# Performance work log

Measured on AMD Instinct MI355X. Metric: run time of the kernel, lower is better.

Reference implementation:

```python
import jax, jax.numpy as jnp
import numpy as np

EPS = 1e-12  # F.normalize default eps


def setup_inputs() -> dict:
    key = jax.random.key(0)
    k1, k2, k3, k4 = jax.random.split(key, 4)
    b, n, c, h = 8, 4096, 768, 8
    scale = 1.0 / np.sqrt(c)
    return {
        "x": jax.random.normal(k1, (b, n, c), dtype=jnp.float32),
        "W_qkv": jax.random.normal(k2, (c, 3 * c), dtype=jnp.float32) * scale,
        "W_proj": jax.random.normal(k3, (c, c), dtype=jnp.float32) * scale,
        "b_proj": jax.random.normal(k4, (c,), dtype=jnp.float32) * 0.01,
        "temperature": jnp.ones((h, 1, 1), dtype=jnp.float32),
    }


def _l2norm(t):
    # F.normalize(t, dim=-1): t / max(||t||_2, eps)
    nrm = jnp.sqrt(jnp.sum(t * t, axis=-1, keepdims=True))
    return t / jnp.maximum(nrm, EPS)


def reference(x, W_qkv, W_proj, b_proj, temperature):
    b, n, c = x.shape
    h = temperature.shape[0]
    d = c // h  # head_dim
    # qkv: (b, n, 3c) -> (b, n, 3, h, d) -> (3, b, h, d, n)
    qkv = (x @ W_qkv).reshape(b, n, 3, h, d).transpose(2, 0, 3, 4, 1)
    q, k, v = qkv[0], qkv[1], qkv[2]  # each (b, h, d, n)
    qn = _l2norm(q)
    kn = _l2norm(k)
    # cross-covariance attention: (b, h, d, d)
    attn = jnp.einsum('bhdn,bhen->bhde', qn, kn) * temperature
    attn = jax.nn.softmax(attn, axis=-1)
    out = jnp.einsum('bhde,bhen->bhdn', attn, v)  # (b, h, d, n)
    out = out.transpose(0, 3, 1, 2).reshape(b, n, c)
    return out @ W_proj + b_proj
```

## Files before the change

### kernel.cpp

```cpp
#include <hip/hip_runtime.h>
#include <math.h>

#define NB  8
#define SEQ 4096
#define CH  768
#define NH  8
#define HD  96
#define NC3 2304

typedef _Float16 f16x8 __attribute__((ext_vector_type(8)));
typedef float    f32x4 __attribute__((ext_vector_type(4)));

static const size_t XT_B   = 0;
static const size_t UT_B   = 0;
static const size_t ATT_B  = 28311552;
static const size_t MT_B   = 29491200;
static const size_t PT_B   = 38928384;
static const size_t GP_B   = 50331648;
static const size_t XH_B   = 50331648;
static const size_t WH_B   = 100663296;
static const size_t WT_B   = 104202240;
static const size_t WPT_B  = 107741184;
static const size_t G_B    = 108920832;
static const size_t INV_B  = 118358016;

__device__ __forceinline__ void gload16(const void* g, void* l) {
  __builtin_amdgcn_global_load_lds(
      (const __attribute__((address_space(1))) void*)g,
      (__attribute__((address_space(3))) void*)l, 16, 0, 0);
}

__global__ void cvt_f16_kernel(const float* __restrict__ in,
                               _Float16* __restrict__ out, int n4) {
  int i = blockIdx.x * blockDim.x + threadIdx.x;
  if (i < n4) {
    float4 v = *(const float4*)(in + (size_t)i * 4);
    _Float16* o = out + (size_t)i * 4;
    o[0] = (_Float16)v.x; o[1] = (_Float16)v.y;
    o[2] = (_Float16)v.z; o[3] = (_Float16)v.w;
  }
}

__global__ void transpose_cvt_kernel(const float* __restrict__ in,
                                     _Float16* __restrict__ outT,
                                     int R, int C, long sIn, long sOut) {
  __shared__ float t[32][33];
  const int b = blockIdx.z;
  const int c0 = blockIdx.x * 32, r0 = blockIdx.y * 32;
  const int tx = threadIdx.x & 31, ty = threadIdx.x >> 5;
  const float* ib = in + (size_t)b * sIn;
  _Float16* ob = outT + (size_t)b * sOut;
#pragma unroll
  for (int k = 0; k < 4; ++k)
    t[ty + 8 * k][tx] = ib[(size_t)(r0 + ty + 8 * k) * C + c0 + tx];
  __syncthreads();
#pragma unroll
  for (int k = 0; k < 4; ++k)
    ob[(size_t)(c0 + ty + 8 * k) * R + r0 + tx] = (_Float16)t[tx][ty + 8 * k];
}

template<bool FP16OUT, bool BIAS, bool TRI>
__global__ __launch_bounds__(256) void gemm_bt_mfma(
    const _Float16* __restrict__ Ap, const _Float16* __restrict__ Bp,
    const float* __restrict__ bias, void* __restrict__ Cp,
    int K, int lda, int ldb, int ldc,
    long sA, long sB, long sC, int zdiv, long aCS, long bCS, long cCS,
    int gx, int gy) {
  __shared__ __align__(16) _Float16 ldsA[2][128 * 32];
  __shared__ __align__(16) _Float16 ldsB[2][128 * 32];

  const int nwg = gridDim.x;
  const int lid = blockIdx.x;
  const int wg = (lid & 7) * (nwg >> 3) + (lid >> 3);
  int bx, by, z;
  if constexpr (TRI) {
    int tt = wg % 21; z = wg / 21;
    int ti = 0, rem = tt;
    while (rem >= 6 - ti) { rem -= 6 - ti; ++ti; }
    by = ti; bx = ti + rem;
  } else {
    bx = wg % gx; int r2 = wg / gx; by = r2 % gy; z = r2 / gy;
  }
  const int bat = z % zdiv, chk = z / zdiv;
  const _Float16* A = Ap + (size_t)bat * sA + (size_t)chk * aCS;
  const _Float16* B = Bp + (size_t)bat * sB + (size_t)chk * bCS;
  const size_t cOff = (size_t)bat * sC + (size_t)chk * cCS;

  const int row0 = by * 128, col0 = bx * 128;
  const int tid = threadIdx.x;
  const int l = tid & 63, w = tid >> 6;
  const int lo = l & 15, hi = l >> 4;
  const int wr = w >> 1, wc = w & 1;

  const int rw = 32 * w;
  const int lr = l >> 2;
  const int ls = l & 3;

  f32x4 acc[4][4];
#pragma unroll
  for (int i = 0; i < 4; ++i)
#pragma unroll
    for (int j = 0; j < 4; ++j)
      acc[i][j] = (f32x4){0.f, 0.f, 0.f, 0.f};

  auto STAGE = [&](int hb, int k0) {
#pragma unroll
    for (int q = 0; q < 2; ++q) {
      const int r = rw + 16 * q + lr;
      const int ck = ls ^ ((r >> 1) & 3);
      gload16(A + (size_t)(row0 + r) * lda + k0 + 8 * ck,
              &ldsA[hb][(rw + 16 * q) * 32]);
      gload16(B + (size_t)(col0 + r) * ldb + k0 + 8 * ck,
              &ldsB[hb][(rw + 16 * q) * 32]);
    }
  };

  STAGE(0, 0);
  const int nt = K / 32;
  int cur = 0;
  for (int t = 0; t < nt; ++t) {
    if (t + 1 < nt) {
      STAGE(cur ^ 1, 32 * (t + 1));
      asm volatile("s_waitcnt vmcnt(4)" : : : "memory");
    } else {
      asm volatile("s_waitcnt vmcnt(0)" : : : "memory");
    }
    __builtin_amdgcn_s_barrier();

    f16x8 a[4], b[4];
#pragma unroll
    for (int mi = 0; mi < 4; ++mi) {
      int Ra = 64 * wr + 16 * mi + lo;
      a[mi] = *(const f16x8*)&ldsA[cur][Ra * 32 + (hi ^ ((Ra >> 1) & 3)) * 8];
    }
#pragma unroll
    for (int ni = 0; ni < 4; ++ni) {
      int Rb = 64 * wc + 16 * ni + lo;
      b[ni] = *(const f16x8*)&ldsB[cur][Rb * 32 + (hi ^ ((Rb >> 1) & 3)) * 8];
    }
#pragma unroll
    for (int mi = 0; mi < 4; ++mi)
#pragma unroll
      for (int ni = 0; ni < 4; ++ni)
        acc[mi][ni] = __builtin_amdgcn_mfma_f32_16x16x32_f16(
            a[mi], b[ni], acc[mi][ni], 0, 0, 0);

    __builtin_amdgcn_s_barrier();
    cur ^= 1;
  }

#pragma unroll
  for (int ni = 0; ni < 4; ++ni) {
    const int col = col0 + 64 * wc + 16 * ni + lo;
    float bv = 0.f;
    if constexpr (BIAS) bv = bias[col];
#pragma unroll
    for (int mi = 0; mi < 4; ++mi) {
      const int rowb = row0 + 64 * wr + 16 * mi + 4 * hi;
#pragma unroll
      for (int r = 0; r < 4; ++r) {
        float v = acc[mi][ni][r] + bv;
        if constexpr (FP16OUT)
          ((_Float16*)Cp)[cOff + (size_t)(rowb + r) * ldc + col] = (_Float16)v;
        else
          ((float*)Cp)[cOff + (size_t)(rowb + r) * ldc + col] = v;
      }
    }
  }
}

__global__ void reduce_mirror_kernel(const _Float16* __restrict__ GP,
                                     _Float16* __restrict__ G) {
  const int t = blockIdx.x, b = blockIdx.y;
  int ti = 0, rem = t;
  while (rem >= 6 - ti) { rem -= 6 - ti; ++ti; }
  const int tj = ti + rem;
  const int i0 = ti * 128, j0 = tj * 128;
  const int tx = threadIdx.x & 31, ty = threadIdx.x >> 5;
  __shared__ float lds[32][33];
  const size_t cs = (size_t)NB * CH * CH;
  const _Float16* gp = GP + (size_t)b * CH * CH;
  _Float16* g = G + (size_t)b * CH * CH;

  for (int st = 0; st < 16; ++st) {
    const int sr = i0 + (st >> 2) * 32, sc = j0 + (st & 3) * 32;
    __syncthreads();
#pragma unroll
    for (int k = 0; k < 4; ++k) {
      const int r = ty + 8 * k;
      const size_t off = (size_t)(sr + r) * CH + sc + tx;
      float v = ((float)gp[off] + (float)gp[cs + off]) +
                ((float)gp[2 * cs + off] + (float)gp[3 * cs + off]);
      lds[r][tx] = v;
      g[off] = (_Float16)v;
    }
    if (ti != tj) {
      __syncthreads();
#pragma unroll
      for (int k = 0; k < 4; ++k) {
        const int r = ty + 8 * k;
        g[(size_t)(sc + r) * CH + sr + tx] = (_Float16)lds[tx][r];
      }
    }
  }
}

__global__ void norm_kernel(const _Float16* __restrict__ Ut,
                            const _Float16* __restrict__ Wt,
                            float* __restrict__ INVv) {
  const int z = blockIdx.x;
  const int t = z >> 3;
  const int c = blockIdx.y * 128 + threadIdx.x;
  const _Float16* u = Ut + ((size_t)z * CH + c) * CH;
  const _Float16* wv = Wt + ((size_t)(t * CH + c)) * CH;
  float s = 0.f;
  for (int i = 0; i < CH; i += 8) {
    f16x8 uv = *(const f16x8*)(u + i);
    f16x8 wq = *(const f16x8*)(wv + i);
#pragma unroll
    for (int q = 0; q < 8; ++q) s += (float)uv[q] * (float)wq[q];
  }
  s = fmaxf(s, 0.f);
  INVv[(size_t)z * CH + c] = 1.0f / fmaxf(sqrtf(s), 1e-12f);
}

__global__ __launch_bounds__(256) void sattn_kernel(
    const _Float16* __restrict__ WT_, const _Float16* __restrict__ UT_,
    const float* __restrict__ INVv, const float* __restrict__ temp,
    _Float16* __restrict__ ATt) {
  const int bh = blockIdx.x;
  const int b = bh >> 3, h = bh & 7;
  __shared__ __align__(16) _Float16 lds[2][192 * 32];
  __shared__ float S[96][100];

  const int tid = threadIdx.x;
  const int l = tid & 63, w = tid >> 6;
  const int lo = l & 15, hi = l >> 4;
  const int wr = w >> 1, wc = w & 1;
  const int lr = l >> 2, lq = l & 3;

  const _Float16* Abase = WT_ + (size_t)(h * HD) * CH;
  const _Float16* Bbase = UT_ + ((size_t)(8 + b) * CH + h * HD) * CH;

  f32x4 acc[3][3];
#pragma unroll
  for (int i = 0; i < 3; ++i)
#pragma unroll
    for (int j = 0; j < 3; ++j)
      acc[i][j] = (f32x4){0.f, 0.f, 0.f, 0.f};

  auto STAGE = [&](int hb, int k0) {
#pragma unroll
    for (int c = 0; c < 3; ++c) {
      const int group = w * 3 + c;
      const int row = group * 16 + lr;
      const int ck = lq ^ ((row >> 1) & 3);
      const _Float16* src = (row < 96)
          ? Abase + (size_t)row * CH + k0 + 8 * ck
          : Bbase + (size_t)(row - 96) * CH + k0 + 8 * ck;
      gload16(src, &lds[hb][group * 512]);
    }
  };

  STAGE(0, 0);
  int cur = 0;
  for (int t = 0; t < 24; ++t) {
    if (t + 1 < 24) {
      STAGE(cur ^ 1, 32 * (t + 1));
      asm volatile("s_waitcnt vmcnt(3)" : : : "memory");
    } else {
      asm volatile("s_waitcnt vmcnt(0)" : : : "memory");
    }
    __builtin_amdgcn_s_barrier();

    f16x8 a[3], bb[3];
#pragma unroll
    for (int mi = 0; mi < 3; ++mi) {
      const int Ra = 48 * wr + 16 * mi + lo;
      a[mi] = *(const f16x8*)&lds[cur][Ra * 32 + (hi ^ ((Ra >> 1) & 3)) * 8];
    }
#pragma unroll
    for (int ni = 0; ni < 3; ++ni) {
      const int Rb = 96 + 48 * wc + 16 * ni + lo;
      bb[ni] = *(const f16x8*)&lds[cur][Rb * 32 + (hi ^ ((Rb >> 1) & 3)) * 8];
    }
#pragma unroll
    for (int mi = 0; mi < 3; ++mi)
#pragma unroll
      for (int ni = 0; ni < 3; ++ni)
        acc[mi][ni] = __builtin_amdgcn_mfma_f32_16x16x32_f16(
            a[mi], bb[ni], acc[mi][ni], 0, 0, 0);

    __builtin_amdgcn_s_barrier();
    cur ^= 1;
  }

  const float tv = temp[h];
  const float* iq = INVv + (size_t)b * CH + h * HD;
  const float* ik = INVv + (size_t)(8 + b) * CH + h * HD;
#pragma unroll
  for (int ni = 0; ni < 3; ++ni) {
    const int col = 48 * wc + 16 * ni + lo;
    const float ikv = ik[col];
#pragma unroll
    for (int mi = 0; mi < 3; ++mi) {
      const int rb = 48 * wr + 16 * mi + 4 * hi;
#pragma unroll
      for (int r = 0; r < 4; ++r)
        S[rb + r][col] = acc[mi][ni][r] * iq[rb + r] * ikv * tv;
    }
  }
  __syncthreads();

  const int g16 = tid >> 4, l16 = tid & 15;
  _Float16* ab = ATt + (size_t)bh * 9216;
#pragma unroll
  for (int it = 0; it < 6; ++it) {
    const int d = g16 + 16 * it;
    float v[6];
    float mx = -INFINITY;
#pragma unroll
    for (int j = 0; j < 6; ++j) { v[j] = S[d][l16 * 6 + j]; mx = fmaxf(mx, v[j]); }
#pragma unroll
    for (int m = 1; m < 16; m <<= 1) mx = fmaxf(mx, __shfl_xor(mx, m, 16));
    float sum = 0.f;
#pragma unroll
    for (int j = 0; j < 6; ++j) { v[j] = __expf(v[j] - mx); sum += v[j]; }
#pragma unroll
    for (int m = 1; m < 16; m <<= 1) sum += __shfl_xor(sum, m, 16);
    const float inv = 1.0f / sum;
#pragma unroll
    for (int j = 0; j < 6; ++j)
      ab[(size_t)(l16 * 6 + j) * 96 + d] = (_Float16)(v[j] * inv);
  }
}

__global__ void mt_kernel(const _Float16* __restrict__ Wpt,
                          const _Float16* __restrict__ ATt,
                          _Float16* __restrict__ Mt) {
  const int j0 = blockIdx.x * 128;
  const int bh = blockIdx.y;
  const int b = bh >> 3, h = bh & 7;
  const int tx = threadIdx.x & 15, ty = threadIdx.x >> 4;
  __shared__ float Ws[16][128], Ats[16][96];
  float acc[8][6] = {};

  for (int d0 = 0; d0 < 96; d0 += 16) {
    {
      int jj = threadIdx.x >> 1, s8 = (threadIdx.x & 1) * 8;
      f16x8 v = *(const f16x8*)(Wpt + (size_t)(j0 + jj) * CH + h * HD + d0 + s8);
#pragma unroll
      for (int q = 0; q < 8; ++q) Ws[s8 + q][jj] = (float)v[q];
    }
    if (threadIdx.x < 192) {
      int e = threadIdx.x >> 1, s8 = (threadIdx.x & 1) * 8;
      f16x8 v = *(const f16x8*)(ATt + (size_t)bh * 9216 + (size_t)e * 96 + d0 + s8);
#pragma unroll
      for (int q = 0; q < 8; ++q) Ats[s8 + q][e] = (float)v[q];
    }
    __syncthreads();
#pragma unroll
    for (int kk = 0; kk < 16; ++kk) {
      float a[8], bb[6];
#pragma unroll
      for (int i = 0; i < 8; ++i) a[i] = Ws[kk][ty * 8 + i];
#pragma unroll
      for (int j = 0; j < 6; ++j) bb[j] = Ats[kk][tx * 6 + j];
#pragma unroll
      for (int i = 0; i < 8; ++i)
#pragma unroll
        for (int j = 0; j < 6; ++j)
          acc[i][j] += a[i] * bb[j];
    }
    __syncthreads();
  }

  _Float16* mb = Mt + (size_t)b * CH * CH;
#pragma unroll
  for (int i = 0; i < 8; ++i)
#pragma unroll
    for (int j = 0; j < 6; ++j)
      mb[(size_t)(j0 + ty * 8 + i) * CH + h * HD + tx * 6 + j] = (_Float16)acc[i][j];
}

extern "C" void kernel_launch(void* const* d_in, const int* in_sizes, int n_in,
                              void* d_out, int out_size, void* d_ws, size_t ws_size,
                              hipStream_t stream) {
  const float* x      = (const float*)d_in[0];
  const float* W_qkv  = (const float*)d_in[1];
  const float* W_proj = (const float*)d_in[2];
  const float* b_proj = (const float*)d_in[3];
  const float* temp   = (const float*)d_in[4];
  float* out = (float*)d_out;
  char* ws = (char*)d_ws;

  _Float16* XT  = (_Float16*)(ws + XT_B);
  _Float16* UT  = (_Float16*)(ws + UT_B);
  _Float16* ATT = (_Float16*)(ws + ATT_B);
  _Float16* MT  = (_Float16*)(ws + MT_B);
  _Float16* PT  = (_Float16*)(ws + PT_B);
  _Float16* GP  = (_Float16*)(ws + GP_B);
  _Float16* XH  = (_Float16*)(ws + XH_B);
  _Float16* WH  = (_Float16*)(ws + WH_B);
  _Float16* WT  = (_Float16*)(ws + WT_B);
  _Float16* WPT = (_Float16*)(ws + WPT_B);
  _Float16* G   = (_Float16*)(ws + G_B);
  float*    INV = (float*)   (ws + INV_B);

  const long CC = (long)CH * CH;
  const long SC = (long)SEQ * CH;

  cvt_f16_kernel<<<(CH * NC3 / 4 + 255) / 256, 256, 0, stream>>>(
      W_qkv, WH, CH * NC3 / 4);
  transpose_cvt_kernel<<<dim3(CH / 32, SEQ / 32, NB), 256, 0, stream>>>(
      x, XT, SEQ, CH, SC, SC);
  transpose_cvt_kernel<<<dim3(NC3 / 32, CH / 32, 1), 256, 0, stream>>>(
      W_qkv, WT, CH, NC3, 0, 0);
  transpose_cvt_kernel<<<dim3(CH / 32, CH / 32, 1), 256, 0, stream>>>(
      W_proj, WPT, CH, CH, 0, 0);

  gemm_bt_mfma<true, false, true><<<672, 256, 0, stream>>>(
      XT, XT, nullptr, GP, 1024, SEQ, SEQ, CH,
      (long)CH * SEQ, (long)CH * SEQ, CC, NB, 1024, 1024, (long)NB * CC,
      21, 1);

  reduce_mirror_kernel<<<dim3(21, NB), 256, 0, stream>>>(GP, G);

  gemm_bt_mfma<true, false, false><<<576, 256, 0, stream>>>(
      WT, G, nullptr, UT, CH, CH, CH, CH,
      0, CC, CC, NB, CC, 0, (long)NB * CC, 6, 6);

  norm_kernel<<<dim3(16, 6), 128, 0, stream>>>(UT, WT, INV);

  sattn_kernel<<<64, 256, 0, stream>>>(WT, UT, INV, temp, ATT);

  mt_kernel<<<dim3(6, 64), 256, 0, stream>>>(WPT, ATT, MT);

  gemm_bt_mfma<true, false, false><<<288, 256, 0, stream>>>(
      MT, WH + 2 * CH, nullptr, PT, CH, CH, NC3, CH,
      CC, 0, CC, NB, 0, 0, 0, 6, 6);

  cvt_f16_kernel<<<(int)(NB * SC / 4 / 256), 256, 0, stream>>>(
      x, XH, (int)(NB * SC / 4));

  gemm_bt_mfma<false, true, false><<<1536, 256, 0, stream>>>(
      XH, PT, b_proj, out, CH, CH, CH, CH,
      SC, CC, SC, NB, 0, 0, 0, 6, 32);
}
```

Before: 265.2 us.

## Add 256x256 MFMA GEMM tile and fuse fp16 copy of x into transpose

Adds a 512-thread GEMM kernel with 256x256 output tiles and K=64 stages. Its loads for the next stage are interleaved with MFMA sub-blocks inside one tile, and it replaces the 128x128 kernel for the Gram, U and final projection GEMMs. The reduce_mirror triangle tiling is adjusted to match. When the workspace is large enough, the transpose kernel also writes a row-major fp16 copy of x, which removes the separate conversion pass over x. Larger tiles improve operand reuse but give far fewer workgroups (192, 144 and 384), which risks underfilling the GPU's compute units and raises register pressure.

```diff
diff --git a/kernel.cpp b/kernel.cpp
--- a/kernel.cpp
+++ b/kernel.cpp
@@ -23,6 +23,8 @@
 static const size_t WPT_B  = 107741184;
 static const size_t G_B    = 108920832;
 static const size_t INV_B  = 118358016;
+static const size_t XH2_B  = 118407168;
+static const size_t XH_BYTES = (size_t)NB * SEQ * CH * 2;
 
 __device__ __forceinline__ void gload16(const void* g, void* l) {
   __builtin_amdgcn_global_load_lds(
@@ -43,6 +45,7 @@
 
 __global__ void transpose_cvt_kernel(const float* __restrict__ in,
                                      _Float16* __restrict__ outT,
+                                     _Float16* __restrict__ outH,
                                      int R, int C, long sIn, long sOut) {
   __shared__ float t[32][33];
   const int b = blockIdx.z;
@@ -51,8 +54,12 @@
   const float* ib = in + (size_t)b * sIn;
   _Float16* ob = outT + (size_t)b * sOut;
 #pragma unroll
-  for (int k = 0; k < 4; ++k)
-    t[ty + 8 * k][tx] = ib[(size_t)(r0 + ty + 8 * k) * C + c0 + tx];
+  for (int k = 0; k < 4; ++k) {
+    float v = ib[(size_t)(r0 + ty + 8 * k) * C + c0 + tx];
+    t[ty + 8 * k][tx] = v;
+    if (outH)
+      outH[(size_t)b * sOut + (size_t)(r0 + ty + 8 * k) * C + c0 + tx] = (_Float16)v;
+  }
   __syncthreads();
 #pragma unroll
   for (int k = 0; k < 4; ++k)
@@ -60,7 +67,175 @@
 }
 
 template<bool FP16OUT, bool BIAS, bool TRI>
-__global__ __launch_bounds__(256) void gemm_bt_mfma(
+__global__ __launch_bounds__(512) void gemm_bt_256(
+    const _Float16* __restrict__ Ap, const _Float16* __restrict__ Bp,
+    const float* __restrict__ bias, void* __restrict__ Cp,
+    int K, int lda, int ldb, int ldc,
+    long sA, long sB, long sC, int zdiv, long aCS, long bCS, long cCS,
+    int gx, int gy) {
+  __shared__ __align__(16) _Float16 lds[2][2][256 * 64];
+
+  const int nwg = gridDim.x;
+  const int lid = blockIdx.x;
+  const int wg = (lid & 7) * (nwg >> 3) + (lid >> 3);
+  int bx, by, z;
+  if constexpr (TRI) {
+    const int ntri = gx * (gx + 1) / 2;
+    int tt = wg % ntri; z = wg / ntri;
+    int ti = 0, rem = tt;
+    while (rem >= gx - ti) { rem -= gx - ti; ++ti; }
+    by = ti; bx = ti + rem;
+  } else {
+    bx = wg % gx; int r2 = wg / gx; by = r2 % gy; z = r2 / gy;
+  }
+  const int bat = z % zdiv, chk = z / zdiv;
+  const _Float16* A = Ap + (size_t)bat * sA + (size_t)chk * aCS;
+  const _Float16* B = Bp + (size_t)bat * sB + (size_t)chk * bCS;
+  const size_t cOff = (size_t)bat * sC + (size_t)chk * cCS;
+
+  const int row0 = by * 256, col0 = bx * 256;
+  const int tid = threadIdx.x;
+  const int l = tid & 63, w = tid >> 6;
+  const int lo = l & 15, hi = l >> 4;
+  const int wr = w >> 2, wc = w & 3;
+
+  const int srow = l >> 3;
+  const int sslot = l & 7;
+
+  f32x4 acc[8][4];
+#pragma unroll
+  for (int i = 0; i < 8; ++i)
+#pragma unroll
+    for (int j = 0; j < 4; ++j)
+      acc[i][j] = (f32x4){0.f, 0.f, 0.f, 0.f};
+
+  auto STAGE_A = [&](int buf, int k0, int c) {
+    const int r = 32 * w + 8 * c + srow;
+    const int ck = sslot ^ (r & 7);
+    gload16(A + (size_t)(row0 + r) * lda + k0 + 8 * ck,
+            &lds[buf][0][(32 * w + 8 * c) * 64]);
+  };
+  auto STAGE_B = [&](int buf, int k0, int c) {
+    const int r = 32 * w + 8 * c + srow;
+    const int ck = sslot ^ (r & 7);
+    gload16(B + (size_t)(col0 + r) * ldb + k0 + 8 * ck,
+            &lds[buf][1][(32 * w + 8 * c) * 64]);
+  };
+  auto LDA_f = [&](int buf, int mi, int kk) -> f16x8 {
+    const int R = 128 * wr + 16 * mi + lo;
+    const int sl = (kk * 4 + hi) ^ (R & 7);
+    return *(const f16x8*)&lds[buf][0][R * 64 + sl * 8];
+  };
+  auto LDB_f = [&](int buf, int ni, int kk) -> f16x8 {
+    const int R = 64 * wc + 16 * ni + lo;
+    const int sl = (kk * 4 + hi) ^ (R & 7);
+    return *(const f16x8*)&lds[buf][1][R * 64 + sl * 8];
+  };
+
+#pragma unroll
+  for (int c = 0; c < 4; ++c) STAGE_A(0, 0, c);
+#pragma unroll
+  for (int c = 0; c < 4; ++c) STAGE_B(0, 0, c);
+  asm volatile("s_waitcnt vmcnt(0)" ::: "memory");
+  __builtin_amdgcn_s_barrier();
+
+  const int nt = K / 64;
+  int cur = 0;
+  f16x8 a[4][2], b0[2][2], b1[2][2];
+
+  for (int t = 0; t < nt; ++t) {
+    const int nx = cur ^ 1;
+    const bool pre = (t + 1 < nt);
+    const int k1 = 64 * (t + 1);
+
+#pragma unroll
+    for (int mi = 0; mi < 4; ++mi) {
+      a[mi][0] = LDA_f(cur, mi, 0); a[mi][1] = LDA_f(cur, mi, 1);
+    }
+#pragma unroll
+    for (int ni = 0; ni < 2; ++ni) {
+      b0[ni][0] = LDB_f(cur, ni, 0); b0[ni][1] = LDB_f(cur, ni, 1);
+    }
+    if (pre) { STAGE_A(nx, k1, 0); STAGE_A(nx, k1, 1); }
+    __builtin_amdgcn_s_barrier();
+#pragma unroll
+    for (int mi = 0; mi < 4; ++mi)
+#pragma unroll
+      for (int ni = 0; ni < 2; ++ni)
+#pragma unroll
+        for (int kk = 0; kk < 2; ++kk)
+          acc[mi][ni] = __builtin_amdgcn_mfma_f32_16x16x32_f16(
+              a[mi][kk], b0[ni][kk], acc[mi][ni], 0, 0, 0);
+    __builtin_amdgcn_s_barrier();
+
+#pragma unroll
+    for (int ni = 0; ni < 2; ++ni) {
+      b1[ni][0] = LDB_f(cur, ni + 2, 0); b1[ni][1] = LDB_f(cur, ni + 2, 1);
+    }
+    if (pre) { STAGE_A(nx, k1, 2); STAGE_A(nx, k1, 3); }
+    __builtin_amdgcn_s_barrier();
+#pragma unroll
+    for (int mi = 0; mi < 4; ++mi)
+#pragma unroll
+      for (int ni = 0; ni < 2; ++ni)
+#pragma unroll
+        for (int kk = 0; kk < 2; ++kk)
+          acc[mi][ni + 2] = __builtin_amdgcn_mfma_f32_16x16x32_f16(
+              a[mi][kk], b1[ni][kk], acc[mi][ni + 2], 0, 0, 0);
+    __builtin_amdgcn_s_barrier();
+
+#pragma unroll
+    for (int mi = 0; mi < 4; ++mi) {
+      a[mi][0] = LDA_f(cur, mi + 4, 0); a[mi][1] = LDA_f(cur, mi + 4, 1);
+    }
+    if (pre) { STAGE_B(nx, k1, 0); STAGE_B(nx, k1, 1); }
+    __builtin_amdgcn_s_barrier();
+#pragma unroll
+    for (int mi = 0; mi < 4; ++mi)
+#pragma unroll
+      for (int ni = 0; ni < 2; ++ni)
+#pragma unroll
+        for (int kk = 0; kk < 2; ++kk)
+          acc[mi + 4][ni] = __builtin_amdgcn_mfma_f32_16x16x32_f16(
+              a[mi][kk], b0[ni][kk], acc[mi + 4][ni], 0, 0, 0);
+    __builtin_amdgcn_s_barrier();
+
+    if (pre) { STAGE_B(nx, k1, 2); STAGE_B(nx, k1, 3); }
+#pragma unroll
+    for (int mi = 0; mi < 4; ++mi)
+#pragma unroll
+      for (int ni = 0; ni < 2; ++ni)
+#pragma unroll
+        for (int kk = 0; kk < 2; ++kk)
+          acc[mi + 4][ni + 2] = __builtin_amdgcn_mfma_f32_16x16x32_f16(
+              a[mi][kk], b1[ni][kk], acc[mi + 4][ni + 2], 0, 0, 0);
+    asm volatile("s_waitcnt vmcnt(0)" ::: "memory");
+    __builtin_amdgcn_s_barrier();
+    cur = nx;
+  }
+
+#pragma unroll
+  for (int ni = 0; ni < 4; ++ni) {
+    const int col = col0 + 64 * wc + 16 * ni + lo;
+    float bv = 0.f;
+    if constexpr (BIAS) bv = bias[col];
+#pragma unroll
+    for (int mi = 0; mi < 8; ++mi) {
+      const int rowb = row0 + 128 * wr + 16 * mi + 4 * hi;
+#pragma unroll
+      for (int r = 0; r < 4; ++r) {
+        float v = acc[mi][ni][r] + bv;
+        if constexpr (FP16OUT)
+          ((_Float16*)Cp)[cOff + (size_t)(rowb + r) * ldc + col] = (_Float16)v;
+        else
+          ((float*)Cp)[cOff + (size_t)(rowb + r) * ldc + col] = v;
+      }
+    }
+  }
+}
+
+template<bool FP16OUT, bool BIAS>
+__global__ __launch_bounds__(256) void gemm_bt_128(
     const _Float16* __restrict__ Ap, const _Float16* __restrict__ Bp,
     const float* __restrict__ bias, void* __restrict__ Cp,
     int K, int lda, int ldb, int ldc,
@@ -72,15 +247,7 @@
   const int nwg = gridDim.x;
   const int lid = blockIdx.x;
   const int wg = (lid & 7) * (nwg >> 3) + (lid >> 3);
-  int bx, by, z;
-  if constexpr (TRI) {
-    int tt = wg % 21; z = wg / 21;
-    int ti = 0, rem = tt;
-    while (rem >= 6 - ti) { rem -= 6 - ti; ++ti; }
-    by = ti; bx = ti + rem;
-  } else {
-    bx = wg % gx; int r2 = wg / gx; by = r2 % gy; z = r2 / gy;
-  }
+  int bx = wg % gx; int r2 = wg / gx; int by = r2 % gy; int z = r2 / gy;
   const int bat = z % zdiv, chk = z / zdiv;
   const _Float16* A = Ap + (size_t)bat * sA + (size_t)chk * aCS;
   const _Float16* B = Bp + (size_t)bat * sB + (size_t)chk * bCS;
@@ -91,7 +258,6 @@
   const int l = tid & 63, w = tid >> 6;
   const int lo = l & 15, hi = l >> 4;
   const int wr = w >> 1, wc = w & 1;
-
   const int rw = 32 * w;
   const int lr = l >> 2;
   const int ls = l & 3;
@@ -121,9 +287,9 @@
   for (int t = 0; t < nt; ++t) {
     if (t + 1 < nt) {
       STAGE(cur ^ 1, 32 * (t + 1));
-      asm volatile("s_waitcnt vmcnt(4)" : : : "memory");
+      asm volatile("s_waitcnt vmcnt(4)" ::: "memory");
     } else {
-      asm volatile("s_waitcnt vmcnt(0)" : : : "memory");
+      asm volatile("s_waitcnt vmcnt(0)" ::: "memory");
     }
     __builtin_amdgcn_s_barrier();
 
@@ -173,17 +339,17 @@
                                      _Float16* __restrict__ G) {
   const int t = blockIdx.x, b = blockIdx.y;
   int ti = 0, rem = t;
-  while (rem >= 6 - ti) { rem -= 6 - ti; ++ti; }
+  while (rem >= 3 - ti) { rem -= 3 - ti; ++ti; }
   const int tj = ti + rem;
-  const int i0 = ti * 128, j0 = tj * 128;
+  const int i0 = ti * 256, j0 = tj * 256;
   const int tx = threadIdx.x & 31, ty = threadIdx.x >> 5;
   __shared__ float lds[32][33];
   const size_t cs = (size_t)NB * CH * CH;
   const _Float16* gp = GP + (size_t)b * CH * CH;
   _Float16* g = G + (size_t)b * CH * CH;
 
-  for (int st = 0; st < 16; ++st) {
-    const int sr = i0 + (st >> 2) * 32, sc = j0 + (st & 3) * 32;
+  for (int st = 0; st < 64; ++st) {
+    const int sr = i0 + (st >> 3) * 32, sc = j0 + (st & 7) * 32;
     __syncthreads();
 #pragma unroll
     for (int k = 0; k < 4; ++k) {
@@ -267,9 +433,9 @@
   for (int t = 0; t < 24; ++t) {
     if (t + 1 < 24) {
       STAGE(cur ^ 1, 32 * (t + 1));
-      asm volatile("s_waitcnt vmcnt(3)" : : : "memory");
+      asm volatile("s_waitcnt vmcnt(3)" ::: "memory");
     } else {
-      asm volatile("s_waitcnt vmcnt(0)" : : : "memory");
+      asm volatile("s_waitcnt vmcnt(0)" ::: "memory");
     }
     __builtin_amdgcn_s_barrier();
 
@@ -407,28 +573,31 @@
   _Float16* G   = (_Float16*)(ws + G_B);
   float*    INV = (float*)   (ws + INV_B);
 
+  const bool fast = ws_size >= XH2_B + XH_BYTES;
+  _Float16* XHU = fast ? (_Float16*)(ws + XH2_B) : XH;
+
   const long CC = (long)CH * CH;
   const long SC = (long)SEQ * CH;
 
   cvt_f16_kernel<<<(CH * NC3 / 4 + 255) / 256, 256, 0, stream>>>(
       W_qkv, WH, CH * NC3 / 4);
   transpose_cvt_kernel<<<dim3(CH / 32, SEQ / 32, NB), 256, 0, stream>>>(
-      x, XT, SEQ, CH, SC, SC);
+      x, XT, fast ? XHU : nullptr, SEQ, CH, SC, SC);
   transpose_cvt_kernel<<<dim3(NC3 / 32, CH / 32, 1), 256, 0, stream>>>(
-      W_qkv, WT, CH, NC3, 0, 0);
+      W_qkv, WT, nullptr, CH, NC3, 0, 0);
   transpose_cvt_kernel<<<dim3(CH / 32, CH / 32, 1), 256, 0, stream>>>(
-      W_proj, WPT, CH, CH, 0, 0);
-
-  gemm_bt_mfma<true, false, true><<<672, 256, 0, stream>>>(
+      W_proj, WPT, nullptr, CH, CH, 0, 0);
+
+  gemm_bt_256<true, false, true><<<192, 512, 0, stream>>>(
       XT, XT, nullptr, GP, 1024, SEQ, SEQ, CH,
       (long)CH * SEQ, (long)CH * SEQ, CC, NB, 1024, 1024, (long)NB * CC,
-      21, 1);
-
-  reduce_mirror_kernel<<<dim3(21, NB), 256, 0, stream>>>(GP, G);
-
-  gemm_bt_mfma<true, false, false><<<576, 256, 0, stream>>>(
+      3, 1);
+
+  reduce_mirror_kernel<<<dim3(6, NB), 256, 0, stream>>>(GP, G);
+
+  gemm_bt_256<true, false, false><<<144, 512, 0, stream>>>(
       WT, G, nullptr, UT, CH, CH, CH, CH,
-      0, CC, CC, NB, CC, 0, (long)NB * CC, 6, 6);
+      0, CC, CC, NB, CC, 0, (long)NB * CC, 3, 3);
 
   norm_kernel<<<dim3(16, 6), 128, 0, stream>>>(UT, WT, INV);
 
@@ -436,14 +605,15 @@
 
   mt_kernel<<<dim3(6, 64), 256, 0, stream>>>(WPT, ATT, MT);
 
-  gemm_bt_mfma<true, false, false><<<288, 256, 0, stream>>>(
+  gemm_bt_128<true, false><<<288, 256, 0, stream>>>(
       MT, WH + 2 * CH, nullptr, PT, CH, CH, NC3, CH,
       CC, 0, CC, NB, 0, 0, 0, 6, 6);
 
-  cvt_f16_kernel<<<(int)(NB * SC / 4 / 256), 256, 0, stream>>>(
-      x, XH, (int)(NB * SC / 4));
-
-  gemm_bt_mfma<false, true, false><<<1536, 256, 0, stream>>>(
-      XH, PT, b_proj, out, CH, CH, CH, CH,
-      SC, CC, SC, NB, 0, 0, 0, 6, 32);
-}
+  if (!fast)
+    cvt_f16_kernel<<<(int)(NB * SC / 4 / 256), 256, 0, stream>>>(
+        x, XH, (int)(NB * SC / 4));
+
+  gemm_bt_256<false, true, false><<<384, 512, 0, stream>>>(
+      XHU, PT, b_proj, out, CH, CH, CH, CH,
+      SC, CC, SC, NB, 0, 0, 0, 3, 16);
+}
```

After: 307.9 us. 16.1% more time.

## Fuse x fp16 conversion into transpose and add 256-row wide GEMM tiles

Applied to the files above, without the earlier changes.

The transpose kernel for x now also writes a row-major fp16 copy into a separate workspace region, so the standalone fp16 conversion pass over x can be skipped when the workspace is large enough. A new 512-thread GEMM variant with 256x128 tiles replaces the 128x128 kernel for the U and final projection GEMMs. This halves the workgroup count and reuses each B tile across more rows. The wide tiles raise LDS use per workgroup, and the fast path depends on the workspace size.

```diff
diff --git a/kernel.cpp b/kernel.cpp
--- a/kernel.cpp
+++ b/kernel.cpp
@@ -23,6 +23,8 @@
 static const size_t WPT_B  = 107741184;
 static const size_t G_B    = 108920832;
 static const size_t INV_B  = 118358016;
+static const size_t XH2_B  = 118407168;
+static const size_t XH_BYTES = (size_t)NB * SEQ * CH * 2;
 
 __device__ __forceinline__ void gload16(const void* g, void* l) {
   __builtin_amdgcn_global_load_lds(
@@ -43,6 +45,7 @@
 
 __global__ void transpose_cvt_kernel(const float* __restrict__ in,
                                      _Float16* __restrict__ outT,
+                                     _Float16* __restrict__ outH,
                                      int R, int C, long sIn, long sOut) {
   __shared__ float t[32][33];
   const int b = blockIdx.z;
@@ -51,8 +54,12 @@
   const float* ib = in + (size_t)b * sIn;
   _Float16* ob = outT + (size_t)b * sOut;
 #pragma unroll
-  for (int k = 0; k < 4; ++k)
-    t[ty + 8 * k][tx] = ib[(size_t)(r0 + ty + 8 * k) * C + c0 + tx];
+  for (int k = 0; k < 4; ++k) {
+    float v = ib[(size_t)(r0 + ty + 8 * k) * C + c0 + tx];
+    t[ty + 8 * k][tx] = v;
+    if (outH)
+      outH[(size_t)b * sOut + (size_t)(r0 + ty + 8 * k) * C + c0 + tx] = (_Float16)v;
+  }
   __syncthreads();
 #pragma unroll
   for (int k = 0; k < 4; ++k)
@@ -91,7 +98,6 @@
   const int l = tid & 63, w = tid >> 6;
   const int lo = l & 15, hi = l >> 4;
   const int wr = w >> 1, wc = w & 1;
-
   const int rw = 32 * w;
   const int lr = l >> 2;
   const int ls = l & 3;
@@ -121,9 +127,114 @@
   for (int t = 0; t < nt; ++t) {
     if (t + 1 < nt) {
       STAGE(cur ^ 1, 32 * (t + 1));
-      asm volatile("s_waitcnt vmcnt(4)" : : : "memory");
+      asm volatile("s_waitcnt vmcnt(4)" ::: "memory");
     } else {
-      asm volatile("s_waitcnt vmcnt(0)" : : : "memory");
+      asm volatile("s_waitcnt vmcnt(0)" ::: "memory");
+    }
+    __builtin_amdgcn_s_barrier();
+
+    f16x8 a[4], b[4];
+#pragma unroll
+    for (int mi = 0; mi < 4; ++mi) {
+      int Ra = 64 * wr + 16 * mi + lo;
+      a[mi] = *(const f16x8*)&ldsA[cur][Ra * 32 + (hi ^ ((Ra >> 1) & 3)) * 8];
+    }
+#pragma unroll
+    for (int ni = 0; ni < 4; ++ni) {
+      int Rb = 64 * wc + 16 * ni + lo;
+      b[ni] = *(const f16x8*)&ldsB[cur][Rb * 32 + (hi ^ ((Rb >> 1) & 3)) * 8];
+    }
+#pragma unroll
+    for (int mi = 0; mi < 4; ++mi)
+#pragma unroll
+      for (int ni = 0; ni < 4; ++ni)
+        acc[mi][ni] = __builtin_amdgcn_mfma_f32_16x16x32_f16(
+            a[mi], b[ni], acc[mi][ni], 0, 0, 0);
+
+    __builtin_amdgcn_s_barrier();
+    cur ^= 1;
+  }
+
+#pragma unroll
+  for (int ni = 0; ni < 4; ++ni) {
+    const int col = col0 + 64 * wc + 16 * ni + lo;
+    float bv = 0.f;
+    if constexpr (BIAS) bv = bias[col];
+#pragma unroll
+    for (int mi = 0; mi < 4; ++mi) {
+      const int rowb = row0 + 64 * wr + 16 * mi + 4 * hi;
+#pragma unroll
+      for (int r = 0; r < 4; ++r) {
+        float v = acc[mi][ni][r] + bv;
+        if constexpr (FP16OUT)
+          ((_Float16*)Cp)[cOff + (size_t)(rowb + r) * ldc + col] = (_Float16)v;
+        else
+          ((float*)Cp)[cOff + (size_t)(rowb + r) * ldc + col] = v;
+      }
+    }
+  }
+}
+
+template<bool FP16OUT, bool BIAS>
+__global__ __launch_bounds__(512) void gemm_bt_wide(
+    const _Float16* __restrict__ Ap, const _Float16* __restrict__ Bp,
+    const float* __restrict__ bias, void* __restrict__ Cp,
+    int K, int lda, int ldb, int ldc,
+    long sA, long sB, long sC, int zdiv, long aCS, long bCS, long cCS,
+    int gx, int gy) {
+  __shared__ __align__(16) _Float16 ldsA[2][256 * 32];
+  __shared__ __align__(16) _Float16 ldsB[2][128 * 32];
+
+  const int nwg = gridDim.x;
+  const int lid = blockIdx.x;
+  const int wg = (lid & 7) * (nwg >> 3) + (lid >> 3);
+  int bx = wg % gx; int r2 = wg / gx; int by = r2 % gy; int z = r2 / gy;
+  const int bat = z % zdiv, chk = z / zdiv;
+  const _Float16* A = Ap + (size_t)bat * sA + (size_t)chk * aCS;
+  const _Float16* B = Bp + (size_t)bat * sB + (size_t)chk * bCS;
+  const size_t cOff = (size_t)bat * sC + (size_t)chk * cCS;
+
+  const int row0 = by * 256, col0 = bx * 128;
+  const int tid = threadIdx.x;
+  const int l = tid & 63, w = tid >> 6;
+  const int lo = l & 15, hi = l >> 4;
+  const int wr = w >> 1, wc = w & 1;
+  const int rw = 32 * w;
+  const int lr = l >> 2;
+  const int ls = l & 3;
+
+  f32x4 acc[4][4];
+#pragma unroll
+  for (int i = 0; i < 4; ++i)
+#pragma unroll
+    for (int j = 0; j < 4; ++j)
+      acc[i][j] = (f32x4){0.f, 0.f, 0.f, 0.f};
+
+  auto STAGE = [&](int hb, int k0) {
+#pragma unroll
+    for (int q = 0; q < 2; ++q) {
+      const int r = rw + 16 * q + lr;
+      const int ck = ls ^ ((r >> 1) & 3);
+      gload16(A + (size_t)(row0 + r) * lda + k0 + 8 * ck,
+              &ldsA[hb][(rw + 16 * q) * 32]);
+      if (w < 4)
+        gload16(B + (size_t)(col0 + r) * ldb + k0 + 8 * ck,
+                &ldsB[hb][(rw + 16 * q) * 32]);
+    }
+  };
+
+  STAGE(0, 0);
+  const int nt = K / 32;
+  int cur = 0;
+  for (int t = 0; t < nt; ++t) {
+    if (t + 1 < nt) {
+      STAGE(cur ^ 1, 32 * (t + 1));
+      if (w < 4)
+        asm volatile("s_waitcnt vmcnt(4)" ::: "memory");
+      else
+        asm volatile("s_waitcnt vmcnt(2)" ::: "memory");
+    } else {
+      asm volatile("s_waitcnt vmcnt(0)" ::: "memory");
     }
     __builtin_amdgcn_s_barrier();
 
@@ -267,9 +378,9 @@
   for (int t = 0; t < 24; ++t) {
     if (t + 1 < 24) {
       STAGE(cur ^ 1, 32 * (t + 1));
-      asm volatile("s_waitcnt vmcnt(3)" : : : "memory");
+      asm volatile("s_waitcnt vmcnt(3)" ::: "memory");
     } else {
-      asm volatile("s_waitcnt vmcnt(0)" : : : "memory");
+      asm volatile("s_waitcnt vmcnt(0)" ::: "memory");
     }
     __builtin_amdgcn_s_barrier();
 
@@ -407,17 +518,20 @@
   _Float16* G   = (_Float16*)(ws + G_B);
   float*    INV = (float*)   (ws + INV_B);
 
+  const bool fast = ws_size >= XH2_B + XH_BYTES;
+  _Float16* XHU = fast ? (_Float16*)(ws + XH2_B) : XH;
+
   const long CC = (long)CH * CH;
   const long SC = (long)SEQ * CH;
 
   cvt_f16_kernel<<<(CH * NC3 / 4 + 255) / 256, 256, 0, stream>>>(
       W_qkv, WH, CH * NC3 / 4);
   transpose_cvt_kernel<<<dim3(CH / 32, SEQ / 32, NB), 256, 0, stream>>>(
-      x, XT, SEQ, CH, SC, SC);
+      x, XT, fast ? XHU : nullptr, SEQ, CH, SC, SC);
   transpose_cvt_kernel<<<dim3(NC3 / 32, CH / 32, 1), 256, 0, stream>>>(
-      W_qkv, WT, CH, NC3, 0, 0);
+      W_qkv, WT, nullptr, CH, NC3, 0, 0);
   transpose_cvt_kernel<<<dim3(CH / 32, CH / 32, 1), 256, 0, stream>>>(
-      W_proj, WPT, CH, CH, 0, 0);
+      W_proj, WPT, nullptr, CH, CH, 0, 0);
 
   gemm_bt_mfma<true, false, true><<<672, 256, 0, stream>>>(
       XT, XT, nullptr, GP, 1024, SEQ, SEQ, CH,
@@ -426,9 +540,9 @@
 
   reduce_mirror_kernel<<<dim3(21, NB), 256, 0, stream>>>(GP, G);
 
-  gemm_bt_mfma<true, false, false><<<576, 256, 0, stream>>>(
+  gemm_bt_wide<true, false><<<288, 512, 0, stream>>>(
       WT, G, nullptr, UT, CH, CH, CH, CH,
-      0, CC, CC, NB, CC, 0, (long)NB * CC, 6, 6);
+      0, CC, CC, NB, CC, 0, (long)NB * CC, 6, 3);
 
   norm_kernel<<<dim3(16, 6), 128, 0, stream>>>(UT, WT, INV);
 
@@ -440,10 +554,11 @@
       MT, WH + 2 * CH, nullptr, PT, CH, CH, NC3, CH,
       CC, 0, CC, NB, 0, 0, 0, 6, 6);
 
-  cvt_f16_kernel<<<(int)(NB * SC / 4 / 256), 256, 0, stream>>>(
-      x, XH, (int)(NB * SC / 4));
-
-  gemm_bt_mfma<false, true, false><<<1536, 256, 0, stream>>>(
-      XH, PT, b_proj, out, CH, CH, CH, CH,
-      SC, CC, SC, NB, 0, 0, 0, 6, 32);
-}
+  if (!fast)
+    cvt_f16_kernel<<<(int)(NB * SC / 4 / 256), 256, 0, stream>>>(
+        x, XH, (int)(NB * SC / 4));
+
+  gemm_bt_wide<false, true><<<768, 512, 0, stream>>>(
+      XHU, PT, b_proj, out, CH, CH, CH, CH,
+      SC, CC, SC, NB, 0, 0, 0, 6, 16);
+}
```

Result: slower. 274.7 us (+3.6%).

## Triple-buffer GEMM LDS pipeline and fuse x fp16 copy into transpose

Applied to the files above, without the earlier changes.

The MFMA GEMM moves from double- to triple-buffered LDS staging with a prefetch distance of two k-tiles, giving global loads more time to land before compute. The x transpose kernel now also writes a row-major fp16 copy of x, which removes the separate full-size cvt pass over x when the workspace is large enough. The extra LDS per block (48KB instead of 32KB) may reduce occupancy. The fused path needs a larger workspace and falls back to the old path otherwise.

```diff
diff --git a/kernel.cpp b/kernel.cpp
--- a/kernel.cpp
+++ b/kernel.cpp
@@ -23,6 +23,8 @@
 static const size_t WPT_B  = 107741184;
 static const size_t G_B    = 108920832;
 static const size_t INV_B  = 118358016;
+static const size_t XH2_B  = 118407168;
+static const size_t XH_BYTES = (size_t)NB * SEQ * CH * 2;
 
 __device__ __forceinline__ void gload16(const void* g, void* l) {
   __builtin_amdgcn_global_load_lds(
@@ -43,6 +45,7 @@
 
 __global__ void transpose_cvt_kernel(const float* __restrict__ in,
                                      _Float16* __restrict__ outT,
+                                     _Float16* __restrict__ outH,
                                      int R, int C, long sIn, long sOut) {
   __shared__ float t[32][33];
   const int b = blockIdx.z;
@@ -51,8 +54,12 @@
   const float* ib = in + (size_t)b * sIn;
   _Float16* ob = outT + (size_t)b * sOut;
 #pragma unroll
-  for (int k = 0; k < 4; ++k)
-    t[ty + 8 * k][tx] = ib[(size_t)(r0 + ty + 8 * k) * C + c0 + tx];
+  for (int k = 0; k < 4; ++k) {
+    float v = ib[(size_t)(r0 + ty + 8 * k) * C + c0 + tx];
+    t[ty + 8 * k][tx] = v;
+    if (outH)
+      outH[(size_t)b * sOut + (size_t)(r0 + ty + 8 * k) * C + c0 + tx] = (_Float16)v;
+  }
   __syncthreads();
 #pragma unroll
   for (int k = 0; k < 4; ++k)
@@ -66,8 +73,8 @@
     int K, int lda, int ldb, int ldc,
     long sA, long sB, long sC, int zdiv, long aCS, long bCS, long cCS,
     int gx, int gy) {
-  __shared__ __align__(16) _Float16 ldsA[2][128 * 32];
-  __shared__ __align__(16) _Float16 ldsB[2][128 * 32];
+  __shared__ __align__(16) _Float16 ldsA[3][128 * 32];
+  __shared__ __align__(16) _Float16 ldsB[3][128 * 32];
 
   const int nwg = gridDim.x;
   const int lid = blockIdx.x;
@@ -91,7 +98,6 @@
   const int l = tid & 63, w = tid >> 6;
   const int lo = l & 15, hi = l >> 4;
   const int wr = w >> 1, wc = w & 1;
-
   const int rw = 32 * w;
   const int lr = l >> 2;
   const int ls = l & 3;
@@ -115,15 +121,19 @@
     }
   };
 
+  const int nt = K / 32;
   STAGE(0, 0);
-  const int nt = K / 32;
+  if (nt > 1) STAGE(1, 32);
   int cur = 0;
   for (int t = 0; t < nt; ++t) {
-    if (t + 1 < nt) {
-      STAGE(cur ^ 1, 32 * (t + 1));
-      asm volatile("s_waitcnt vmcnt(4)" : : : "memory");
+    if (t + 2 < nt) {
+      int n2 = cur + 2; if (n2 >= 3) n2 -= 3;
+      STAGE(n2, 32 * (t + 2));
+      asm volatile("s_waitcnt vmcnt(8)" ::: "memory");
+    } else if (t + 1 < nt) {
+      asm volatile("s_waitcnt vmcnt(4)" ::: "memory");
     } else {
-      asm volatile("s_waitcnt vmcnt(0)" : : : "memory");
+      asm volatile("s_waitcnt vmcnt(0)" ::: "memory");
     }
     __builtin_amdgcn_s_barrier();
 
@@ -146,7 +156,7 @@
             a[mi], b[ni], acc[mi][ni], 0, 0, 0);
 
     __builtin_amdgcn_s_barrier();
-    cur ^= 1;
+    ++cur; if (cur == 3) cur = 0;
   }
 
 #pragma unroll
@@ -267,9 +277,9 @@
   for (int t = 0; t < 24; ++t) {
     if (t + 1 < 24) {
       STAGE(cur ^ 1, 32 * (t + 1));
-      asm volatile("s_waitcnt vmcnt(3)" : : : "memory");
+      asm volatile("s_waitcnt vmcnt(3)" ::: "memory");
     } else {
-      asm volatile("s_waitcnt vmcnt(0)" : : : "memory");
+      asm volatile("s_waitcnt vmcnt(0)" ::: "memory");
     }
     __builtin_amdgcn_s_barrier();
 
@@ -407,17 +417,20 @@
   _Float16* G   = (_Float16*)(ws + G_B);
   float*    INV = (float*)   (ws + INV_B);
 
+  const bool fast = ws_size >= XH2_B + XH_BYTES;
+  _Float16* XHU = fast ? (_Float16*)(ws + XH2_B) : XH;
+
   const long CC = (long)CH * CH;
   const long SC = (long)SEQ * CH;
 
   cvt_f16_kernel<<<(CH * NC3 / 4 + 255) / 256, 256, 0, stream>>>(
       W_qkv, WH, CH * NC3 / 4);
   transpose_cvt_kernel<<<dim3(CH / 32, SEQ / 32, NB), 256, 0, stream>>>(
-      x, XT, SEQ, CH, SC, SC);
+      x, XT, fast ? XHU : nullptr, SEQ, CH, SC, SC);
   transpose_cvt_kernel<<<dim3(NC3 / 32, CH / 32, 1), 256, 0, stream>>>(
-      W_qkv, WT, CH, NC3, 0, 0);
+      W_qkv, WT, nullptr, CH, NC3, 0, 0);
   transpose_cvt_kernel<<<dim3(CH / 32, CH / 32, 1), 256, 0, stream>>>(
-      W_proj, WPT, CH, CH, 0, 0);
+      W_proj, WPT, nullptr, CH, CH, 0, 0);
 
   gemm_bt_mfma<true, false, true><<<672, 256, 0, stream>>>(
       XT, XT, nullptr, GP, 1024, SEQ, SEQ, CH,
@@ -440,10 +453,11 @@
       MT, WH + 2 * CH, nullptr, PT, CH, CH, NC3, CH,
       CC, 0, CC, NB, 0, 0, 0, 6, 6);
 
-  cvt_f16_kernel<<<(int)(NB * SC / 4 / 256), 256, 0, stream>>>(
-      x, XH, (int)(NB * SC / 4));
+  if (!fast)
+    cvt_f16_kernel<<<(int)(NB * SC / 4 / 256), 256, 0, stream>>>(
+        x, XH, (int)(NB * SC / 4));
 
   gemm_bt_mfma<false, true, false><<<1536, 256, 0, stream>>>(
-      XH, PT, b_proj, out, CH, CH, CH, CH,
+      XHU, PT, b_proj, out, CH, CH, CH, CH,
       SC, CC, SC, NB, 0, 0, 0, 6, 32);
 }
```

Result: no change. 266.9 us (+0.7%).
